# Kernel optimization log

Hardware: AMD Instinct MI355X
Metric: run time of the kernel (lower is better)

The kernel has to match this reference:

```python
import jax, jax.numpy as jnp
import numpy as np

D_MODEL = 1024
H = 16
D_K = D_MODEL // H
D_FF = 4096
EPS = 1e-6
NEG = -1e9


def setup_inputs() -> dict:
    key = jax.random.key(0)
    ks = jax.random.split(key, 8)
    B, S = 2, 2048
    src = jax.random.normal(ks[0], (B, S, D_MODEL), dtype=jnp.float32)
    src_mask = jnp.ones((B, 1, 1, S), dtype=jnp.int32)
    sc = 1.0 / np.sqrt(D_MODEL)
    wq = jax.random.normal(ks[1], (D_MODEL, D_MODEL), jnp.float32) * sc
    wk = jax.random.normal(ks[2], (D_MODEL, D_MODEL), jnp.float32) * sc
    wv = jax.random.normal(ks[3], (D_MODEL, D_MODEL), jnp.float32) * sc
    wo = jax.random.normal(ks[4], (D_MODEL, D_MODEL), jnp.float32) * sc
    w1 = jax.random.normal(ks[5], (D_FF, D_MODEL), jnp.float32) * sc
    b1 = jnp.zeros((D_FF,), jnp.float32)
    w2 = jax.random.normal(ks[6], (D_MODEL, D_FF), jnp.float32) * (1.0 / np.sqrt(D_FF))
    b2 = jnp.zeros((D_MODEL,), jnp.float32)
    a1 = jnp.ones((1,), jnp.float32)
    be1 = jnp.zeros((1,), jnp.float32)
    a2 = jnp.ones((1,), jnp.float32)
    be2 = jnp.zeros((1,), jnp.float32)
    return dict(src=src, src_mask=src_mask, wq=wq, wk=wk, wv=wv, wo=wo,
                w1=w1, b1=b1, w2=w2, b2=b2, a1=a1, be1=be1, a2=a2, be2=be2)


def layer_norm(x, alpha, bias):
    # torch: mean + unbiased std (ddof=1), eps added to std
    mean = jnp.mean(x, axis=-1, keepdims=True)
    std = jnp.sqrt(jnp.var(x, axis=-1, keepdims=True, ddof=1))
    return alpha * (x - mean) / (std + EPS) + bias


def mha(x, mask, wq, wk, wv, wo):
    B, S, _ = x.shape
    def split(t):  # [B,S,D] -> [B,H,S,D_K]
        return t.reshape(B, S, H, D_K).transpose(0, 2, 1, 3)
    q = split(x @ wq.T)
    k = split(x @ wk.T)
    v = split(x @ wv.T)
    scores = jnp.einsum('bhqd,bhkd->bhqk', q, k) / np.sqrt(D_K)
    scores = jnp.where(mask == 0, NEG, scores)
    attn = jax.nn.softmax(scores, axis=-1)
    out = jnp.einsum('bhqk,bhkd->bhqd', attn, v)
    out = out.transpose(0, 2, 1, 3).reshape(B, S, D_MODEL)
    return out @ wo.T


def reference(src, src_mask, wq, wk, wv, wo, w1, b1, w2, b2, a1, be1, a2, be2):
    x = layer_norm(src, a1, be1)
    src = src + mha(x, src_mask, wq, wk, wv, wo)
    x = layer_norm(src, a2, be2)
    ff = jax.nn.relu(x @ w1.T + b1) @ w2.T + b2
    return src + ff
```

## Files before the change

kernel.cpp:

```cpp
#include <hip/hip_runtime.h>
#include <hip/hip_bf16.h>

typedef unsigned short u16;
typedef unsigned int u32;
typedef float floatx4 __attribute__((ext_vector_type(4)));
typedef __bf16 bf16x8 __attribute__((ext_vector_type(8)));
typedef u16 ushort4v __attribute__((ext_vector_type(4)));
typedef u16 ushort8v __attribute__((ext_vector_type(8)));

#define DEVI static __device__ __forceinline__

DEVI u16 f2bf(float f) {
    u32 u = __builtin_bit_cast(u32, f);
    u += 0x7fffu + ((u >> 16) & 1u);
    return (u16)(u >> 16);
}
DEVI float bf2f(u16 h) { return __builtin_bit_cast(float, (u32)h << 16); }

DEVI float fexp2(float x) { return __builtin_amdgcn_exp2f(x); }

DEVI void async_cp16(const u16* g, u16* l) {
    __builtin_amdgcn_global_load_lds((const __attribute__((address_space(1))) u32*)g,
                                     (__attribute__((address_space(3))) u32*)l, 16, 0, 0);
}

template<int BM, int BN, int RW, int CW, bool QKV3, int NSPLIT, bool XSWZ,
         bool BIAS, bool RELU, bool RESID, bool OBF16>
__global__ __launch_bounds__(256) void gemm_nt(
    const u16* __restrict__ A,
    const u16* __restrict__ W0, const u16* __restrict__ W1, const u16* __restrict__ W2,
    const float* __restrict__ bias, const float* __restrict__ resid,
    void* __restrict__ o0, void* __restrict__ o1, void* __restrict__ o2,
    void* __restrict__ o3, int K, int lda, int Nper, int NX)
{
    static_assert(RW * CW == 4, "4 waves");
    constexpr int WM = BM / RW, WN = BN / CW;
    constexpr int MI = WM / 16, NI = WN / 16;
    __shared__ __align__(16) u16 As[2][BM * 32];
    __shared__ __align__(16) u16 Bs[2][BN * 32];
    const int tid = threadIdx.x;
    const int w = tid >> 6, lane = tid & 63;
    const int q = lane >> 4, ml = lane & 15;
    const int wr = w / CW, wc = w % CW;
    int bx = blockIdx.x, by = blockIdx.y;
    if (XSWZ) {
        const int gx = gridDim.x, gy = gridDim.y;
        int L = by * gx + bx;
        int xcd = L & 7, s = L >> 3;
        int mb = gy >> 3;
        by = xcd * mb + s % mb;
        bx = s / mb;
    }
    const int m0 = by * BM;
    size_t kbase = 0;
    const u16* W = W0;
    void* outp = o0;
    if (NSPLIT > 1) {
        int part = bx / NX; bx -= part * NX; kbase = (size_t)part * K;
        outp = (part == 0) ? o0 : (part == 1 ? o1 : (part == 2 ? o2 : o3));
    }
    int n0 = bx * BN;
    if (QKV3) {
        int sel = n0 / Nper;
        n0 -= sel * Nper;
        W = (sel == 0) ? W0 : (sel == 1 ? W1 : W2);
        outp = (sel == 0) ? o0 : (sel == 1 ? o1 : o2);
    }

    auto stage = [&](int buf, int kt) {
#pragma unroll
        for (int p = 0; p < BM / 64; ++p) {
            int g = p * 256 + tid;
            int r = g >> 2, s = g & 3;
            int c = s ^ ((r >> 1) & 3);
            async_cp16(A + (size_t)(m0 + r) * lda + kbase + kt + c * 8,
                       &As[buf][(p * 256 + w * 64) * 8]);
        }
#pragma unroll
        for (int p = 0; p < BN / 64; ++p) {
            int g = p * 256 + tid;
            int r = g >> 2, s = g & 3;
            int c = s ^ ((r >> 1) & 3);
            async_cp16(W + (size_t)(n0 + r) * lda + kbase + kt + c * 8,
                       &Bs[buf][(p * 256 + w * 64) * 8]);
        }
    };

    const floatx4 fzero = {0.f, 0.f, 0.f, 0.f};
    floatx4 acc[MI][NI];
#pragma unroll
    for (int i = 0; i < MI; ++i)
#pragma unroll
        for (int j = 0; j < NI; ++j) acc[i][j] = fzero;

    stage(0, 0);
    for (int it = 0, kt = 0; kt < K; ++it, kt += 32) {
        __syncthreads();
        if (kt + 32 < K) stage((it + 1) & 1, kt + 32);
        const u16* Asb = As[it & 1];
        const u16* Bsb = Bs[it & 1];
        bf16x8 af[MI], bfr[NI];
#pragma unroll
        for (int i = 0; i < MI; ++i) {
            int rm = wr * WM + i * 16 + ml;
            int s = q ^ ((rm >> 1) & 3);
            af[i] = *(const bf16x8*)&Asb[(rm * 4 + s) * 8];
        }
#pragma unroll
        for (int j = 0; j < NI; ++j) {
            int rn = wc * WN + j * 16 + ml;
            int s = q ^ ((rn >> 1) & 3);
            bfr[j] = *(const bf16x8*)&Bsb[(rn * 4 + s) * 8];
        }
#pragma unroll
        for (int i = 0; i < MI; ++i)
#pragma unroll
            for (int j = 0; j < NI; ++j)
                acc[i][j] = __builtin_amdgcn_mfma_f32_16x16x32_bf16(af[i], bfr[j], acc[i][j], 0, 0, 0);
    }

#pragma unroll
    for (int j = 0; j < NI; ++j) {
        int gn = n0 + wc * WN + j * 16 + ml;
        float bj = 0.f;
        if (BIAS) bj = bias[gn];
#pragma unroll
        for (int i = 0; i < MI; ++i) {
            int gm0 = m0 + wr * WM + i * 16 + q * 4;
#pragma unroll
            for (int r = 0; r < 4; ++r) {
                size_t idx = (size_t)(gm0 + r) * Nper + gn;
                float v = acc[i][j][r] + bj;
                if (RELU) v = fmaxf(v, 0.f);
                if (RESID) v += resid[idx];
                if (OBF16) ((u16*)outp)[idx] = f2bf(v);
                else       ((float*)outp)[idx] = v;
            }
        }
    }
}

__global__ __launch_bounds__(128, 2) void flash7(
    const u16* __restrict__ Q, const u16* __restrict__ Kg,
    const u16* __restrict__ Vt, const float* __restrict__ biasv,
    u16* __restrict__ O)
{
    __shared__ __align__(16) u16 Ks[2][64 * 64];
    __shared__ __align__(16) u16 Vs[2][64 * 64];
    const int tid = threadIdx.x;
    const int w = tid >> 6, lane = tid & 63;
    const int q = lane >> 4, ml = lane & 15;
    const int b = blockIdx.y >> 4, h = blockIdx.y & 15;
    const size_t rowQ = (size_t)(b * 2048 + blockIdx.x * 64);
    const float KSC = 0.125f * 1.4426950408889634f;
    const floatx4 fzero = {0.f, 0.f, 0.f, 0.f};

    bf16x8 qa[2][2];
#pragma unroll
    for (int qg = 0; qg < 2; ++qg)
#pragma unroll
        for (int c = 0; c < 2; ++c)
            qa[qg][c] = *(const bf16x8*)&Q[(rowQ + w * 32 + qg * 16 + ml) * 1024
                                           + h * 64 + q * 8 + c * 32];

    auto stage = [&](int buf, int s0) {
#pragma unroll
        for (int p = 0; p < 4; ++p) {
            int L = p * 128 + tid;
            int row = L >> 3, sl = L & 7;
            int ch = sl ^ ((row & 3) | (((row >> 3) & 1) << 2));
            async_cp16(Kg + (size_t)(b * 2048 + s0 + row) * 1024 + h * 64 + ch * 8,
                       &Ks[buf][(p * 128 + w * 64) * 8]);
            async_cp16(Vt + (size_t)(b * 1024 + h * 64 + row) * 2048 + s0 + ch * 8,
                       &Vs[buf][(p * 128 + w * 64) * 8]);
        }
    };

    floatx4 oacc[2][4];
    float lsum[2] = {0.f, 0.f};
#pragma unroll
    for (int qg = 0; qg < 2; ++qg)
#pragma unroll
        for (int d = 0; d < 4; ++d) oacc[qg][d] = fzero;

    const int swk = (ml & 3) | (((ml >> 2) & 1) << 2);
    const int swv = (ml & 3) | (((ml >> 3) & 1) << 2);

    stage(0, 0);
    for (int it = 0; it < 32; ++it) {
        __syncthreads();
        if (it + 1 < 32) stage((it + 1) & 1, (it + 1) * 64);
        const u16* Kb = Ks[it & 1];
        const u16* Vb = Vs[it & 1];
        const int s0 = it * 64;

        bf16x8 pfrag[2][2];
#pragma unroll
        for (int g = 0; g < 2; ++g) {
            const int re = g * 32 + ((ml >> 2) << 3) + (ml & 3);
            bf16x8 ke0 = *(const bf16x8*)&Kb[(re + 0) * 64 + ((0 + q) ^ swk) * 8];
            bf16x8 ke1 = *(const bf16x8*)&Kb[(re + 0) * 64 + ((4 + q) ^ swk) * 8];
            bf16x8 ko0 = *(const bf16x8*)&Kb[(re + 4) * 64 + ((0 + q) ^ swk) * 8];
            bf16x8 ko1 = *(const bf16x8*)&Kb[(re + 4) * 64 + ((4 + q) ^ swk) * 8];
            const float4 be = *(const float4*)&biasv[b * 2048 + s0 + g * 32 + q * 8];
            const float4 bo = *(const float4*)&biasv[b * 2048 + s0 + g * 32 + q * 8 + 4];
#pragma unroll
            for (int qg = 0; qg < 2; ++qg) {
                floatx4 te = fzero, to = fzero;
                te = __builtin_amdgcn_mfma_f32_16x16x32_bf16(ke0, qa[qg][0], te, 0, 0, 0);
                te = __builtin_amdgcn_mfma_f32_16x16x32_bf16(ke1, qa[qg][1], te, 0, 0, 0);
                to = __builtin_amdgcn_mfma_f32_16x16x32_bf16(ko0, qa[qg][0], to, 0, 0, 0);
                to = __builtin_amdgcn_mfma_f32_16x16x32_bf16(ko1, qa[qg][1], to, 0, 0, 0);
                float pe0 = fexp2(fmaf(te[0], KSC, be.x));
                float pe1 = fexp2(fmaf(te[1], KSC, be.y));
                float pe2 = fexp2(fmaf(te[2], KSC, be.z));
                float pe3 = fexp2(fmaf(te[3], KSC, be.w));
                float po0 = fexp2(fmaf(to[0], KSC, bo.x));
                float po1 = fexp2(fmaf(to[1], KSC, bo.y));
                float po2 = fexp2(fmaf(to[2], KSC, bo.z));
                float po3 = fexp2(fmaf(to[3], KSC, bo.w));
                lsum[qg] += ((pe0 + pe1) + (pe2 + pe3)) + ((po0 + po1) + (po2 + po3));
                u32 pk[4];
                pk[0] = ((__builtin_bit_cast(u32, pe0) + 0x8000u) >> 16)
                      | ((__builtin_bit_cast(u32, pe1) + 0x8000u) & 0xffff0000u);
                pk[1] = ((__builtin_bit_cast(u32, pe2) + 0x8000u) >> 16)
                      | ((__builtin_bit_cast(u32, pe3) + 0x8000u) & 0xffff0000u);
                pk[2] = ((__builtin_bit_cast(u32, po0) + 0x8000u) >> 16)
                      | ((__builtin_bit_cast(u32, po1) + 0x8000u) & 0xffff0000u);
                pk[3] = ((__builtin_bit_cast(u32, po2) + 0x8000u) >> 16)
                      | ((__builtin_bit_cast(u32, po3) + 0x8000u) & 0xffff0000u);
                pfrag[g][qg] = __builtin_bit_cast(bf16x8, *(uint4*)pk);
            }
        }
#pragma unroll
        for (int dt = 0; dt < 4; ++dt) {
            int vrow = dt * 16 + ml;
#pragma unroll
            for (int g = 0; g < 2; ++g) {
                bf16x8 vf = *(const bf16x8*)&Vb[vrow * 64 + ((g * 4 + q) ^ swv) * 8];
#pragma unroll
                for (int qg = 0; qg < 2; ++qg)
                    oacc[qg][dt] = __builtin_amdgcn_mfma_f32_16x16x32_bf16(
                        vf, pfrag[g][qg], oacc[qg][dt], 0, 0, 0);
            }
        }
    }
#pragma unroll
    for (int qg = 0; qg < 2; ++qg) {
        float ls = lsum[qg];
        ls += __shfl_xor(ls, 16, 64);
        ls += __shfl_xor(ls, 32, 64);
        const float rcp = 1.f / ls;
        const size_t row = rowQ + w * 32 + qg * 16 + ml;
#pragma unroll
        for (int dt = 0; dt < 4; ++dt)
#pragma unroll
            for (int rp = 0; rp < 4; rp += 2) {
                u32 pk = (u32)f2bf(oacc[qg][dt][rp] * rcp)
                       | ((u32)f2bf(oacc[qg][dt][rp + 1] * rcp) << 16);
                *(u32*)&O[row * 1024 + h * 64 + dt * 16 + q * 4 + rp] = pk;
            }
    }
}

__global__ __launch_bounds__(256) void vtrans(const u16* __restrict__ Vb, u16* __restrict__ Vt)
{
    __shared__ __align__(16) u16 T[64 * 72];
    const int tid = threadIdx.x;
    const int ct = blockIdx.x, rt = blockIdx.y;
    const int b = rt >> 5;
    const int s0 = (rt & 31) * 64;
    const int c0 = ct * 64;
#pragma unroll
    for (int p = 0; p < 2; ++p) {
        int slot = p * 256 + tid;
        int lr = slot >> 3, pc = slot & 7;
        bf16x8 v = *(const bf16x8*)&Vb[(size_t)(b * 2048 + s0 + lr) * 1024 + c0 + pc * 8];
        *(bf16x8*)&T[lr * 72 + pc * 8] = v;
    }
    __syncthreads();
#pragma unroll
    for (int p = 0; p < 2; ++p) {
        int slot = p * 256 + tid;
        int dc = slot >> 3, sc0 = (slot & 7) * 8;
        ushort8v o;
#pragma unroll
        for (int j = 0; j < 8; ++j) o[j] = T[(sc0 + j) * 72 + dc];
        *(ushort8v*)&Vt[(size_t)(b * 1024 + c0 + dc) * 2048 + s0 + sc0] = o;
    }
}

DEVI void ln_row(const float* __restrict__ x, float ga, float gb,
                 u16* __restrict__ y, int row, int tid)
{
    const float4 v = ((const float4*)(x + (size_t)row * 1024))[tid];
    float s = v.x + v.y + v.z + v.w;
    float ss = v.x * v.x + v.y * v.y + v.z * v.z + v.w * v.w;
#pragma unroll
    for (int d = 1; d < 64; d <<= 1) { s += __shfl_xor(s, d, 64); ss += __shfl_xor(ss, d, 64); }
    __shared__ float ps[4], pss[4];
    const int w = tid >> 6, lane = tid & 63;
    if (lane == 0) { ps[w] = s; pss[w] = ss; }
    __syncthreads();
    s = ps[0] + ps[1] + ps[2] + ps[3];
    ss = pss[0] + pss[1] + pss[2] + pss[3];
    float mean = s * (1.f / 1024.f);
    float var = fmaxf((ss - s * mean) * (1.f / 1023.f), 0.f);
    float sc = ga / (sqrtf(var) + 1e-6f);
    ushort4v o;
    o[0] = f2bf((v.x - mean) * sc + gb);
    o[1] = f2bf((v.y - mean) * sc + gb);
    o[2] = f2bf((v.z - mean) * sc + gb);
    o[3] = f2bf((v.w - mean) * sc + gb);
    ((ushort4v*)(y + (size_t)row * 1024))[tid] = o;
}

__global__ __launch_bounds__(256) void ln_bf16(const float* __restrict__ x,
    const float* __restrict__ ga, const float* __restrict__ gb, u16* __restrict__ y)
{
    ln_row(x, ga[0], gb[0], y, blockIdx.x, threadIdx.x);
}

__global__ __launch_bounds__(256) void prep(
    const float* __restrict__ wq, const float* __restrict__ wk,
    const float* __restrict__ wv, const float* __restrict__ wo,
    const float* __restrict__ w1, const float* __restrict__ w2,
    u16* __restrict__ wqb, u16* __restrict__ wkb, u16* __restrict__ wvb,
    u16* __restrict__ wob, u16* __restrict__ w1b, u16* __restrict__ w2b,
    const int* __restrict__ m, float* __restrict__ biasv,
    const float* __restrict__ src, const float* __restrict__ a1,
    const float* __restrict__ be1, u16* __restrict__ xln1)
{
    const int bx = blockIdx.x;
    if (bx < 12288) {
        size_t i = (size_t)bx * 256 + threadIdx.x;
        const float* s; u16* d; size_t off;
        if (i < 262144)       { s = wq; d = wqb; off = i; }
        else if (i < 524288)  { s = wk; d = wkb; off = i - 262144; }
        else if (i < 786432)  { s = wv; d = wvb; off = i - 524288; }
        else if (i < 1048576) { s = wo; d = wob; off = i - 786432; }
        else if (i < 2097152) { s = w1; d = w1b; off = i - 1048576; }
        else                  { s = w2; d = w2b; off = i - 2097152; }
        float4 v = ((const float4*)s)[off];
        ushort4v o = {f2bf(v.x), f2bf(v.y), f2bf(v.z), f2bf(v.w)};
        ((ushort4v*)d)[off] = o;
    } else if (bx < 12304) {
        int i = (bx - 12288) * 256 + threadIdx.x;
        biasv[i] = m[i] ? 0.f : -1.442695e9f;
    } else {
        ln_row(src, a1[0], be1[0], xln1, bx - 12304, threadIdx.x);
    }
}

__global__ __launch_bounds__(256) void ff2_fin(
    const u16* __restrict__ p0, const u16* __restrict__ p1,
    const float* __restrict__ b2, const float* __restrict__ resid,
    float* __restrict__ out)
{
    const size_t i = (size_t)blockIdx.x * 256 + threadIdx.x;
    ushort4v a = *(const ushort4v*)&p0[i * 4];
    ushort4v b = *(const ushort4v*)&p1[i * 4];
    float4 r = ((const float4*)resid)[i];
    float4 bb = ((const float4*)b2)[i & 255];
    float4 o;
    o.x = (bf2f(a[0]) + bf2f(b[0])) + r.x + bb.x;
    o.y = (bf2f(a[1]) + bf2f(b[1])) + r.y + bb.y;
    o.z = (bf2f(a[2]) + bf2f(b[2])) + r.z + bb.z;
    o.w = (bf2f(a[3]) + bf2f(b[3])) + r.w + bb.w;
    ((float4*)out)[i] = o;
}

extern "C" void kernel_launch(void* const* d_in, const int* in_sizes, int n_in,
                              void* d_out, int out_size, void* d_ws, size_t ws_size,
                              hipStream_t stream)
{
    const float* src = (const float*)d_in[0];
    const int* msk   = (const int*)d_in[1];
    const float* wq  = (const float*)d_in[2];
    const float* wk  = (const float*)d_in[3];
    const float* wv  = (const float*)d_in[4];
    const float* wo  = (const float*)d_in[5];
    const float* w1  = (const float*)d_in[6];
    const float* b1  = (const float*)d_in[7];
    const float* w2  = (const float*)d_in[8];
    const float* b2  = (const float*)d_in[9];
    const float* a1  = (const float*)d_in[10];
    const float* be1 = (const float*)d_in[11];
    const float* a2  = (const float*)d_in[12];
    const float* be2 = (const float*)d_in[13];
    float* out = (float*)d_out;

    char* ws = (char*)d_ws;
    const size_t MB = (size_t)1 << 20;
    u16* wqb  = (u16*)(ws + 0 * MB);
    u16* wkb  = (u16*)(ws + 2 * MB);
    u16* wvb  = (u16*)(ws + 4 * MB);
    u16* wob  = (u16*)(ws + 6 * MB);
    u16* w1b  = (u16*)(ws + 8 * MB);
    u16* w2b  = (u16*)(ws + 16 * MB);
    u16* xln1 = (u16*)(ws + 24 * MB);
    u16* attn = xln1;
    u16* Qb   = (u16*)(ws + 32 * MB);
    u16* xln2 = Qb;
    u16* Kb   = (u16*)(ws + 40 * MB);
    u16* Vb   = (u16*)(ws + 48 * MB);
    u16* Vt   = (u16*)(ws + 56 * MB);
    float* biasv = (float*)(ws + 64 * MB);
    u16* h1   = (u16*)(ws + 40 * MB);
    float* src2 = (float*)(ws + 72 * MB);
    u16* P0 = (u16*)(ws + 0 * MB);
    u16* P1 = (u16*)(ws + 24 * MB);

    prep<<<16400, 256, 0, stream>>>(wq, wk, wv, wo, w1, w2,
                                    wqb, wkb, wvb, wob, w1b, w2b,
                                    msk, biasv, src, a1, be1, xln1);

    gemm_nt<128, 128, 2, 2, true, 1, true, false, false, false, true><<<dim3(24, 32), 256, 0, stream>>>(
        xln1, wqb, wkb, wvb, nullptr, nullptr, Qb, Kb, Vb, nullptr, 1024, 1024, 1024, 0);

    vtrans<<<dim3(16, 64), 256, 0, stream>>>(Vb, Vt);

    flash7<<<dim3(32, 32), 128, 0, stream>>>(Qb, Kb, Vt, biasv, attn);

    gemm_nt<128, 64, 4, 1, false, 1, true, false, false, true, false><<<dim3(16, 32), 256, 0, stream>>>(
        attn, wob, nullptr, nullptr, nullptr, src, src2, nullptr, nullptr, nullptr,
        1024, 1024, 1024, 0);

    ln_bf16<<<4096, 256, 0, stream>>>(src2, a2, be2, xln2);

    gemm_nt<128, 128, 2, 2, false, 1, true, true, true, false, true><<<dim3(32, 32), 256, 0, stream>>>(
        xln2, w1b, nullptr, nullptr, b1, nullptr, h1, nullptr, nullptr, nullptr,
        1024, 1024, 4096, 0);

    gemm_nt<128, 128, 2, 2, false, 2, true, false, false, false, true><<<dim3(16, 32), 256, 0, stream>>>(
        h1, w2b, nullptr, nullptr, nullptr, nullptr, P0, P1, nullptr, nullptr,
        2048, 4096, 1024, 8);

    ff2_fin<<<4096, 256, 0, stream>>>(P0, P1, b2, src2, out);
}
```

Measured before the change: 352.3 us.

## Split flash attention KV range across two wave pairs with LDS merge

The attention kernel now launches 256 threads per block instead of 128. Two wave pairs each process half of the key/value sequence in 32-key chunks, then merge their partial output accumulators and row sums through shared memory before normalising. This doubles the waves resident per block to improve latency hiding and MFMA utilisation on an attention grid of only 1024 blocks. The cost is an extra reduction pass through LDS, one more barrier, and smaller per-iteration tiles with more loop overhead. The softmax has no running max, so summing the two halves' partial results directly stays correct.

```diff
diff --git a/kernel.cpp b/kernel.cpp
--- a/kernel.cpp
+++ b/kernel.cpp
@@ -140,15 +140,16 @@
     }
 }
 
-__global__ __launch_bounds__(128, 2) void flash7(
+__global__ __launch_bounds__(256, 4) void flash8(
     const u16* __restrict__ Q, const u16* __restrict__ Kg,
     const u16* __restrict__ Vt, const float* __restrict__ biasv,
     u16* __restrict__ O)
 {
-    __shared__ __align__(16) u16 Ks[2][64 * 64];
-    __shared__ __align__(16) u16 Vs[2][64 * 64];
+    __shared__ __align__(16) u16 Ks[2][2][32 * 64];
+    __shared__ __align__(16) u16 Vs[2][2][64 * 32];
     const int tid = threadIdx.x;
     const int w = tid >> 6, lane = tid & 63;
+    const int qw = w & 1, kv = w >> 1;
     const int q = lane >> 4, ml = lane & 15;
     const int b = blockIdx.y >> 4, h = blockIdx.y & 15;
     const size_t rowQ = (size_t)(b * 2048 + blockIdx.x * 64);
@@ -160,19 +161,29 @@
     for (int qg = 0; qg < 2; ++qg)
 #pragma unroll
         for (int c = 0; c < 2; ++c)
-            qa[qg][c] = *(const bf16x8*)&Q[(rowQ + w * 32 + qg * 16 + ml) * 1024
+            qa[qg][c] = *(const bf16x8*)&Q[(rowQ + qw * 32 + qg * 16 + ml) * 1024
                                            + h * 64 + q * 8 + c * 32];
 
-    auto stage = [&](int buf, int s0) {
-#pragma unroll
-        for (int p = 0; p < 4; ++p) {
-            int L = p * 128 + tid;
-            int row = L >> 3, sl = L & 7;
+    auto stage = [&](int buf, int it) {
+        {
+            int row = tid >> 3, sl = tid & 7;
             int ch = sl ^ ((row & 3) | (((row >> 3) & 1) << 2));
-            async_cp16(Kg + (size_t)(b * 2048 + s0 + row) * 1024 + h * 64 + ch * 8,
-                       &Ks[buf][(p * 128 + w * 64) * 8]);
-            async_cp16(Vt + (size_t)(b * 1024 + h * 64 + row) * 2048 + s0 + ch * 8,
-                       &Vs[buf][(p * 128 + w * 64) * 8]);
+#pragma unroll
+            for (int hf = 0; hf < 2; ++hf) {
+                int s0 = hf * 1024 + it * 32;
+                async_cp16(Kg + (size_t)(b * 2048 + s0 + row) * 1024 + h * 64 + ch * 8,
+                           &Ks[hf][buf][(w * 64) * 8]);
+            }
+        }
+        {
+            int row = tid >> 2, sl = tid & 3;
+            int ch = sl ^ ((row >> 1) & 3);
+#pragma unroll
+            for (int hf = 0; hf < 2; ++hf) {
+                int s0 = hf * 1024 + it * 32;
+                async_cp16(Vt + (size_t)(b * 1024 + h * 64 + row) * 2048 + s0 + ch * 8,
+                           &Vs[hf][buf][(w * 64) * 8]);
+            }
         }
     };
 
@@ -184,74 +195,86 @@
         for (int d = 0; d < 4; ++d) oacc[qg][d] = fzero;
 
     const int swk = (ml & 3) | (((ml >> 2) & 1) << 2);
-    const int swv = (ml & 3) | (((ml >> 3) & 1) << 2);
+    const int re = ((ml >> 2) << 3) + (ml & 3);
 
     stage(0, 0);
     for (int it = 0; it < 32; ++it) {
         __syncthreads();
-        if (it + 1 < 32) stage((it + 1) & 1, (it + 1) * 64);
-        const u16* Kb = Ks[it & 1];
-        const u16* Vb = Vs[it & 1];
-        const int s0 = it * 64;
-
-        bf16x8 pfrag[2][2];
-#pragma unroll
-        for (int g = 0; g < 2; ++g) {
-            const int re = g * 32 + ((ml >> 2) << 3) + (ml & 3);
-            bf16x8 ke0 = *(const bf16x8*)&Kb[(re + 0) * 64 + ((0 + q) ^ swk) * 8];
-            bf16x8 ke1 = *(const bf16x8*)&Kb[(re + 0) * 64 + ((4 + q) ^ swk) * 8];
-            bf16x8 ko0 = *(const bf16x8*)&Kb[(re + 4) * 64 + ((0 + q) ^ swk) * 8];
-            bf16x8 ko1 = *(const bf16x8*)&Kb[(re + 4) * 64 + ((4 + q) ^ swk) * 8];
-            const float4 be = *(const float4*)&biasv[b * 2048 + s0 + g * 32 + q * 8];
-            const float4 bo = *(const float4*)&biasv[b * 2048 + s0 + g * 32 + q * 8 + 4];
-#pragma unroll
-            for (int qg = 0; qg < 2; ++qg) {
-                floatx4 te = fzero, to = fzero;
-                te = __builtin_amdgcn_mfma_f32_16x16x32_bf16(ke0, qa[qg][0], te, 0, 0, 0);
-                te = __builtin_amdgcn_mfma_f32_16x16x32_bf16(ke1, qa[qg][1], te, 0, 0, 0);
-                to = __builtin_amdgcn_mfma_f32_16x16x32_bf16(ko0, qa[qg][0], to, 0, 0, 0);
-                to = __builtin_amdgcn_mfma_f32_16x16x32_bf16(ko1, qa[qg][1], to, 0, 0, 0);
-                float pe0 = fexp2(fmaf(te[0], KSC, be.x));
-                float pe1 = fexp2(fmaf(te[1], KSC, be.y));
-                float pe2 = fexp2(fmaf(te[2], KSC, be.z));
-                float pe3 = fexp2(fmaf(te[3], KSC, be.w));
-                float po0 = fexp2(fmaf(to[0], KSC, bo.x));
-                float po1 = fexp2(fmaf(to[1], KSC, bo.y));
-                float po2 = fexp2(fmaf(to[2], KSC, bo.z));
-                float po3 = fexp2(fmaf(to[3], KSC, bo.w));
-                lsum[qg] += ((pe0 + pe1) + (pe2 + pe3)) + ((po0 + po1) + (po2 + po3));
-                u32 pk[4];
-                pk[0] = ((__builtin_bit_cast(u32, pe0) + 0x8000u) >> 16)
-                      | ((__builtin_bit_cast(u32, pe1) + 0x8000u) & 0xffff0000u);
-                pk[1] = ((__builtin_bit_cast(u32, pe2) + 0x8000u) >> 16)
-                      | ((__builtin_bit_cast(u32, pe3) + 0x8000u) & 0xffff0000u);
-                pk[2] = ((__builtin_bit_cast(u32, po0) + 0x8000u) >> 16)
-                      | ((__builtin_bit_cast(u32, po1) + 0x8000u) & 0xffff0000u);
-                pk[3] = ((__builtin_bit_cast(u32, po2) + 0x8000u) >> 16)
-                      | ((__builtin_bit_cast(u32, po3) + 0x8000u) & 0xffff0000u);
-                pfrag[g][qg] = __builtin_bit_cast(bf16x8, *(uint4*)pk);
-            }
+        if (it + 1 < 32) stage((it + 1) & 1, it + 1);
+        const u16* Kb = Ks[kv][it & 1];
+        const u16* Vb = Vs[kv][it & 1];
+        const int s0 = kv * 1024 + it * 32;
+
+        bf16x8 ke0 = *(const bf16x8*)&Kb[(re + 0) * 64 + ((0 + q) ^ swk) * 8];
+        bf16x8 ke1 = *(const bf16x8*)&Kb[(re + 0) * 64 + ((4 + q) ^ swk) * 8];
+        bf16x8 ko0 = *(const bf16x8*)&Kb[(re + 4) * 64 + ((0 + q) ^ swk) * 8];
+        bf16x8 ko1 = *(const bf16x8*)&Kb[(re + 4) * 64 + ((4 + q) ^ swk) * 8];
+        const float4 be = *(const float4*)&biasv[b * 2048 + s0 + q * 8];
+        const float4 bo = *(const float4*)&biasv[b * 2048 + s0 + q * 8 + 4];
+        bf16x8 pfrag[2];
+#pragma unroll
+        for (int qg = 0; qg < 2; ++qg) {
+            floatx4 te = fzero, to = fzero;
+            te = __builtin_amdgcn_mfma_f32_16x16x32_bf16(ke0, qa[qg][0], te, 0, 0, 0);
+            te = __builtin_amdgcn_mfma_f32_16x16x32_bf16(ke1, qa[qg][1], te, 0, 0, 0);
+            to = __builtin_amdgcn_mfma_f32_16x16x32_bf16(ko0, qa[qg][0], to, 0, 0, 0);
+            to = __builtin_amdgcn_mfma_f32_16x16x32_bf16(ko1, qa[qg][1], to, 0, 0, 0);
+            float pe0 = fexp2(fmaf(te[0], KSC, be.x));
+            float pe1 = fexp2(fmaf(te[1], KSC, be.y));
+            float pe2 = fexp2(fmaf(te[2], KSC, be.z));
+            float pe3 = fexp2(fmaf(te[3], KSC, be.w));
+            float po0 = fexp2(fmaf(to[0], KSC, bo.x));
+            float po1 = fexp2(fmaf(to[1], KSC, bo.y));
+            float po2 = fexp2(fmaf(to[2], KSC, bo.z));
+            float po3 = fexp2(fmaf(to[3], KSC, bo.w));
+            lsum[qg] += ((pe0 + pe1) + (pe2 + pe3)) + ((po0 + po1) + (po2 + po3));
+            u32 pk[4];
+            pk[0] = ((__builtin_bit_cast(u32, pe0) + 0x8000u) >> 16)
+                  | ((__builtin_bit_cast(u32, pe1) + 0x8000u) & 0xffff0000u);
+            pk[1] = ((__builtin_bit_cast(u32, pe2) + 0x8000u) >> 16)
+                  | ((__builtin_bit_cast(u32, pe3) + 0x8000u) & 0xffff0000u);
+            pk[2] = ((__builtin_bit_cast(u32, po0) + 0x8000u) >> 16)
+                  | ((__builtin_bit_cast(u32, po1) + 0x8000u) & 0xffff0000u);
+            pk[3] = ((__builtin_bit_cast(u32, po2) + 0x8000u) >> 16)
+                  | ((__builtin_bit_cast(u32, po3) + 0x8000u) & 0xffff0000u);
+            pfrag[qg] = __builtin_bit_cast(bf16x8, *(uint4*)pk);
         }
 #pragma unroll
         for (int dt = 0; dt < 4; ++dt) {
             int vrow = dt * 16 + ml;
-#pragma unroll
-            for (int g = 0; g < 2; ++g) {
-                bf16x8 vf = *(const bf16x8*)&Vb[vrow * 64 + ((g * 4 + q) ^ swv) * 8];
-#pragma unroll
-                for (int qg = 0; qg < 2; ++qg)
-                    oacc[qg][dt] = __builtin_amdgcn_mfma_f32_16x16x32_bf16(
-                        vf, pfrag[g][qg], oacc[qg][dt], 0, 0, 0);
-            }
-        }
-    }
+            bf16x8 vf = *(const bf16x8*)&Vb[vrow * 32 + ((q ^ ((vrow >> 1) & 3)) * 8)];
+#pragma unroll
+            for (int qg = 0; qg < 2; ++qg)
+                oacc[qg][dt] = __builtin_amdgcn_mfma_f32_16x16x32_bf16(
+                    vf, pfrag[qg], oacc[qg][dt], 0, 0, 0);
+        }
+    }
+
+    __syncthreads();
+    float* sO = (float*)&Ks[0][0][0];
+    float* sL = (float*)&Vs[0][0][0];
+    if (kv == 1) {
+#pragma unroll
+        for (int qg = 0; qg < 2; ++qg) {
+            sL[(qw * 2 + qg) * 64 + lane] = lsum[qg];
+#pragma unroll
+            for (int dt = 0; dt < 4; ++dt)
+                *(floatx4*)&sO[((qw * 2 + qg) * 4 + dt) * 256 + lane * 4] = oacc[qg][dt];
+        }
+    }
+    __syncthreads();
+    if (kv == 1) return;
 #pragma unroll
     for (int qg = 0; qg < 2; ++qg) {
+        lsum[qg] += sL[(qw * 2 + qg) * 64 + lane];
+#pragma unroll
+        for (int dt = 0; dt < 4; ++dt)
+            oacc[qg][dt] += *(const floatx4*)&sO[((qw * 2 + qg) * 4 + dt) * 256 + lane * 4];
         float ls = lsum[qg];
         ls += __shfl_xor(ls, 16, 64);
         ls += __shfl_xor(ls, 32, 64);
         const float rcp = 1.f / ls;
-        const size_t row = rowQ + w * 32 + qg * 16 + ml;
+        const size_t row = rowQ + qw * 32 + qg * 16 + ml;
 #pragma unroll
         for (int dt = 0; dt < 4; ++dt)
 #pragma unroll
@@ -420,7 +443,7 @@
 
     vtrans<<<dim3(16, 64), 256, 0, stream>>>(Vb, Vt);
 
-    flash7<<<dim3(32, 32), 128, 0, stream>>>(Qb, Kb, Vt, biasv, attn);
+    flash8<<<dim3(32, 32), 256, 0, stream>>>(Qb, Kb, Vt, biasv, attn);
 
     gemm_nt<128, 64, 4, 1, false, 1, true, false, false, true, false><<<dim3(16, 32), 256, 0, stream>>>(
         attn, wob, nullptr, nullptr, nullptr, src, src2, nullptr, nullptr, nullptr,
```

Result: no change. 357.8 us (+1.6%).
